# Kernel optimization log

Hardware: AMD Instinct MI355X
Metric: run time of the kernel (lower is better)

Reference implementation:

```python
import jax, jax.numpy as jnp
import numpy as np

# Config (matches init_kwargs)
HIDDEN = 1280
NUM_EXPERTS = 16
NUM_SHARED = 2
NUM_ROUTED = NUM_EXPERTS - NUM_SHARED          # 14
TOPK = 6 - NUM_SHARED                           # num_activated - num_shared = 4
INTERMED = int(int(HIDDEN * 4.0) * 0.25)        # 1280
B, S = 2, 2048


def setup_inputs() -> dict:
    key = jax.random.key(0)
    ks = jax.random.split(key, 12)
    sc = 0.02
    x = jax.random.normal(ks[0], (B, S, HIDDEN), dtype=jnp.float32)
    # shared experts, stacked over expert axis
    W1s = jax.random.normal(ks[1], (NUM_SHARED, HIDDEN, INTERMED), dtype=jnp.float32) * sc
    b1s = jnp.zeros((NUM_SHARED, INTERMED), dtype=jnp.float32)
    W2s = jax.random.normal(ks[2], (NUM_SHARED, INTERMED, HIDDEN), dtype=jnp.float32) * sc
    b2s = jnp.zeros((NUM_SHARED, HIDDEN), dtype=jnp.float32)
    # routed experts
    W1r = jax.random.normal(ks[3], (NUM_ROUTED, HIDDEN, INTERMED), dtype=jnp.float32) * sc
    b1r = jnp.zeros((NUM_ROUTED, INTERMED), dtype=jnp.float32)
    W2r = jax.random.normal(ks[4], (NUM_ROUTED, INTERMED, HIDDEN), dtype=jnp.float32) * sc
    b2r = jnp.zeros((NUM_ROUTED, HIDDEN), dtype=jnp.float32)
    # router
    Wr = jax.random.normal(ks[5], (HIDDEN, NUM_ROUTED), dtype=jnp.float32) * sc
    br = jnp.zeros((NUM_ROUTED,), dtype=jnp.float32)
    return {"x": x, "W1s": W1s, "b1s": b1s, "W2s": W2s, "b2s": b2s,
            "W1r": W1r, "b1r": b1r, "W2r": W2r, "b2r": b2r, "Wr": Wr, "br": br}


def _gelu(x):
    return jax.nn.gelu(x, approximate=False)  # torch nn.GELU default is exact erf


def reference(x, W1s, b1s, W2s, b2s, W1r, b1r, W2r, b2r, Wr, br):
    # shared experts: sum_e FFN_e(x)
    hs = _gelu(jnp.einsum('bsh,ehi->ebsi', x, W1s) + b1s[:, None, None, :])
    shared_out = jnp.einsum('ebsi,eih->bsh', hs, W2s) + b2s.sum(0)

    # router: softmax + top-k gates scattered back to dense [B,S,E]
    logits = jnp.einsum('bsh,he->bse', x, Wr) + br
    aff = jax.nn.softmax(logits, axis=-1)
    topk_vals, topk_idx = jax.lax.top_k(aff, TOPK)
    gates = (jax.nn.one_hot(topk_idx, NUM_ROUTED, dtype=aff.dtype)
             * topk_vals[..., None]).sum(axis=-2)  # [B,S,E]

    # naive dense dispatch: every routed expert over all tokens, gate-weighted
    hr = _gelu(jnp.einsum('bsh,ehi->ebsi', x, W1r) + b1r[:, None, None, :])
    expert_out = jnp.einsum('ebsi,eih->ebsh', hr, W2r) + b2r[:, None, None, :]
    routed_out = jnp.einsum('bse,ebsh->bsh', gates, expert_out)

    return shared_out + routed_out + x
```

## Files before the change

kernel.cpp:

```cpp
#include <hip/hip_runtime.h>
#include <hip/hip_bf16.h>
#include <math.h>

#define H      1280
#define NE     16
#define NR     14
#define TK     4
#define T      4096
#define NROWS  24576
#define MAXT   112
#define NT     (H / 64)

typedef __bf16 bf16x8 __attribute__((ext_vector_type(8)));
typedef float  f32x4  __attribute__((ext_vector_type(4)));
typedef unsigned short us8 __attribute__((ext_vector_type(8)));

__device__ __forceinline__ unsigned short f2bf(float f) {
  unsigned int u = __float_as_uint(f);
  u += 0x7fffu + ((u >> 16) & 1u);
  return (unsigned short)(u >> 16);
}
__device__ __forceinline__ float bf2f(unsigned short u) {
  return __uint_as_float(((unsigned int)u) << 16);
}

__device__ __forceinline__ void gll16(const unsigned short* g, unsigned short* l) {
  __builtin_amdgcn_global_load_lds(
      (const __attribute__((address_space(1))) void*)g,
      (__attribute__((address_space(3))) void*)l, 16, 0, 0);
}

__global__ void k_init(int* cnt, int* fill) {
  int i = threadIdx.x;
  if (i < 16) { cnt[i] = 0; fill[i] = 0; }
}

__global__ void k_cast_x(const float* __restrict__ x, unsigned short* __restrict__ xb) {
  int i = blockIdx.x * 256 + threadIdx.x;
  float4 v = reinterpret_cast<const float4*>(x)[i];
  ushort4 b;
  b.x = f2bf(v.x); b.y = f2bf(v.y); b.z = f2bf(v.z); b.w = f2bf(v.w);
  reinterpret_cast<ushort4*>(xb)[i] = b;
}

__global__ void k_transpose(const float* __restrict__ W1s, const float* __restrict__ W2s,
                            const float* __restrict__ W1r, const float* __restrict__ W2r,
                            unsigned short* __restrict__ w1b, unsigned short* __restrict__ w2b) {
  int mat = blockIdx.z;
  int fam = mat >> 4;
  int e   = mat & 15;
  size_t msz = (size_t)H * H;
  const float* src;
  unsigned short* dst;
  if (fam == 0) {
    src = (e < 2) ? W1s + (size_t)e * msz : W1r + (size_t)(e - 2) * msz;
    dst = w1b + (size_t)e * msz;
  } else {
    src = (e < 2) ? W2s + (size_t)e * msz : W2r + (size_t)(e - 2) * msz;
    dst = w2b + (size_t)e * msz;
  }
  __shared__ unsigned short tile[64][72];
  int tx = threadIdx.x & 15;
  int ty = threadIdx.x >> 4;
  int bx = blockIdx.x * 64;
  int by = blockIdx.y * 64;
#pragma unroll
  for (int p = 0; p < 4; p++) {
    int r = p * 16 + ty;
    float4 v = *reinterpret_cast<const float4*>(&src[(size_t)(by + r) * H + bx + tx * 4]);
    tile[tx * 4 + 0][r] = f2bf(v.x);
    tile[tx * 4 + 1][r] = f2bf(v.y);
    tile[tx * 4 + 2][r] = f2bf(v.z);
    tile[tx * 4 + 3][r] = f2bf(v.w);
  }
  __syncthreads();
  int tx8 = threadIdx.x & 7;
  int rr  = threadIdx.x >> 3;
#pragma unroll
  for (int p = 0; p < 2; p++) {
    int n = p * 32 + rr;
    us8 o = *reinterpret_cast<const us8*>(&tile[n][tx8 * 8]);
    *reinterpret_cast<us8*>(&dst[(size_t)(bx + n) * H + by + tx8 * 8]) = o;
  }
}

__global__ void k_router(const float* __restrict__ x, const float* __restrict__ Wr,
                         const float* __restrict__ br,
                         int* __restrict__ topk_e, float* __restrict__ topk_g) {
  int t  = blockIdx.x * 4 + (threadIdx.x >> 6);
  int ln = threadIdx.x & 63;
  float part[NR];
#pragma unroll
  for (int e = 0; e < NR; e++) part[e] = 0.f;
  const float* xr = x + (size_t)t * H;
  for (int k = ln; k < H; k += 64) {
    float xv = xr[k];
    const float* w = Wr + (size_t)k * NR;
#pragma unroll
    for (int e = 0; e < NR; e++) part[e] += xv * w[e];
  }
  float aff[NR];
#pragma unroll
  for (int e = 0; e < NR; e++) {
    float v = part[e];
#pragma unroll
    for (int off = 32; off; off >>= 1) v += __shfl_down(v, off);
    aff[e] = v + br[e];
  }
  if (ln == 0) {
    float mx = aff[0];
#pragma unroll
    for (int e = 1; e < NR; e++) mx = fmaxf(mx, aff[e]);
    float p[NR]; float s = 0.f;
#pragma unroll
    for (int e = 0; e < NR; e++) { p[e] = expf(aff[e] - mx); s += p[e]; }
    float inv = 1.f / s;
    unsigned used = 0;
    for (int j = 0; j < TK; j++) {
      int be = -1; float bv = -1.f;
#pragma unroll
      for (int e = 0; e < NR; e++)
        if (!((used >> e) & 1u) && p[e] > bv) { bv = p[e]; be = e; }
      used |= 1u << be;
      topk_e[t * TK + j] = be;
      topk_g[t * TK + j] = bv * inv;
    }
  }
}

__global__ void k_count(const int* __restrict__ topk_e, int* __restrict__ cnt) {
  __shared__ int hist[NR];
  int tid = threadIdx.x;
  if (tid < NR) hist[tid] = 0;
  __syncthreads();
  int t = blockIdx.x * 256 + tid;
#pragma unroll
  for (int j = 0; j < TK; j++)
    atomicAdd(&hist[topk_e[t * TK + j]], 1);
  __syncthreads();
  if (tid < NR) atomicAdd(&cnt[tid], hist[tid]);
}

__global__ void k_prefix(const int* __restrict__ cnt, int* __restrict__ segbase,
                         int* __restrict__ segcnt, int* __restrict__ tile_seg,
                         int* __restrict__ tile_m0) {
  if (threadIdx.x == 0) {
    int sc[NE];
    sc[0] = T; sc[1] = T;
    for (int e = 0; e < NR; e++) sc[2 + e] = cnt[e];
    int b = 0;
    for (int s = 0; s < NE; s++) { segbase[s] = b; segcnt[s] = sc[s]; b += sc[s]; }
    int nt = 0;
    for (int s = 0; s < NE; s++)
      for (int m = 0; m < sc[s]; m += 256) { tile_seg[nt] = s; tile_m0[nt] = m; nt++; }
    for (int i = nt; i < MAXT; i++) { tile_seg[i] = -1; tile_m0[i] = 0; }
  }
}

__global__ void k_fill(const int* __restrict__ topk_e,
                       const int* __restrict__ segbase, int* __restrict__ fill,
                       int* __restrict__ rowtok, int* __restrict__ tokrow) {
  __shared__ int lhist[NR];
  __shared__ int lbase[NR];
  int tid = threadIdx.x;
  if (tid < NR) lhist[tid] = 0;
  __syncthreads();
  int t = blockIdx.x * 256 + tid;
  rowtok[t]     = t;
  rowtok[T + t] = t;
  int e[TK], off[TK];
#pragma unroll
  for (int j = 0; j < TK; j++) {
    e[j]   = topk_e[t * TK + j];
    off[j] = atomicAdd(&lhist[e[j]], 1);
  }
  __syncthreads();
  if (tid < NR) lbase[tid] = atomicAdd(&fill[tid], lhist[tid]);
  __syncthreads();
#pragma unroll
  for (int j = 0; j < TK; j++) {
    int r = segbase[2 + e[j]] + lbase[e[j]] + off[j];
    rowtok[r] = t;
    tokrow[t * TK + j] = r;
  }
}


template<int MODE>
__global__ __launch_bounds__(512, 2) void k_gemm(
    const unsigned short* __restrict__ Abase,
    const unsigned short* __restrict__ Wb,
    const float* __restrict__ bs, const float* __restrict__ brr,
    const int* __restrict__ rowtok,
    const int* __restrict__ segbase, const int* __restrict__ segcnt,
    const int* __restrict__ tile_seg, const int* __restrict__ tile_m0,
    unsigned short* __restrict__ obuf) {
  int seg = tile_seg[blockIdx.y];
  if (seg < 0) return;
  int m0  = tile_m0[blockIdx.y];
  int cnt = segcnt[seg];
  int n0  = blockIdx.x * 256;
  int sb  = segbase[seg];
  const unsigned short* Bw = Wb + (size_t)seg * H * H;
  const float* bias = (seg < 2) ? bs + (size_t)seg * H : brr + (size_t)(seg - 2) * H;

  __shared__ __align__(16) unsigned short Al[2][256 * 64];
  __shared__ __align__(16) unsigned short Bl[2][256 * 64];

  int tid = threadIdx.x;
  int wv = tid >> 6, ln = tid & 63;
  int rw = (wv & 1) * 128, cw = (wv >> 1) * 64;
  int quad = ln >> 4, l16 = ln & 15;
  int lrow = tid >> 3;
  int ldst = (tid & 7) * 8;
  int lkc  = (((tid & 7) ^ (lrow & 7))) * 8;

  const unsigned short* asrc[4];
  const unsigned short* bsrc[4];
#pragma unroll
  for (int p = 0; p < 4; p++) {
    int row = p * 64 + lrow;
    if (MODE == 0) {
      int gm  = m0 + row;
      int tok = (gm < cnt) ? rowtok[sb + gm] : 0;
      asrc[p] = Abase + (size_t)tok * H + lkc;
    } else {
      int ar = sb + m0 + row;
      if (ar >= NROWS) ar = 0;
      asrc[p] = Abase + (size_t)ar * H + lkc;
    }
    bsrc[p] = Bw + (size_t)(n0 + row) * H + lkc;
  }

  int xsw = (quad ^ (l16 & 7)) * 8;

  f32x4 acc[8][4];
#pragma unroll
  for (int i = 0; i < 8; i++)
#pragma unroll
    for (int j = 0; j < 4; j++) acc[i][j] = (f32x4){0.f, 0.f, 0.f, 0.f};

  auto STAGE = [&](int tt) {
    int kb = tt << 6;
    unsigned short* Ad = &Al[tt & 1][0];
    unsigned short* Bd = &Bl[tt & 1][0];
#pragma unroll
    for (int p = 0; p < 4; p++) {
      int row = p * 64 + lrow;
      gll16(asrc[p] + kb, Ad + row * 64 + ldst);
      gll16(bsrc[p] + kb, Bd + row * 64 + ldst);
    }
  };

  STAGE(0);
  __syncthreads();

  for (int t = 0; t < NT; ++t) {
    if (t + 1 < NT) STAGE(t + 1);
    const unsigned short* Ac = &Al[t & 1][0];
    const unsigned short* Bc = &Bl[t & 1][0];
#pragma unroll
    for (int kk = 0; kk < 64; kk += 32) {
      bf16x8 af[8], bfr[4];
#pragma unroll
      for (int i = 0; i < 8; i++)
        af[i] = *reinterpret_cast<const bf16x8*>(&Ac[(rw + i * 16 + l16) * 64 + (xsw ^ kk)]);
#pragma unroll
      for (int j = 0; j < 4; j++)
        bfr[j] = *reinterpret_cast<const bf16x8*>(&Bc[(cw + j * 16 + l16) * 64 + (xsw ^ kk)]);
#pragma unroll
      for (int i = 0; i < 8; i++)
#pragma unroll
        for (int j = 0; j < 4; j++)
          acc[i][j] = __builtin_amdgcn_mfma_f32_16x16x32_bf16(af[i], bfr[j], acc[i][j], 0, 0, 0);
    }
    __syncthreads();
  }

#pragma unroll
  for (int i = 0; i < 8; i++) {
#pragma unroll
    for (int r = 0; r < 4; r++) {
      int m = m0 + rw + i * 16 + quad * 4 + r;
      if (m >= cnt) continue;
      size_t ro = (size_t)(sb + m) * H;
#pragma unroll
      for (int j = 0; j < 4; j++) {
        int n = n0 + cw + j * 16 + l16;
        float v = acc[i][j][r] + bias[n];
        if (MODE == 0) {
          float g = 0.5f * v * (1.f + erff(v * 0.70710678118654752f));
          obuf[ro + n] = f2bf(g);
        } else {
          obuf[ro + n] = f2bf(v);
        }
      }
    }
  }
}

__global__ void k_combine(const float* __restrict__ x, const unsigned short* __restrict__ rbuf,
                          const int* __restrict__ tokrow, const float* __restrict__ topk_g,
                          float* __restrict__ out) {
  int i = blockIdx.x * 256 + threadIdx.x;
  int t = i / (H / 4);
  int c = (i - t * (H / 4)) * 4;
  size_t xo = (size_t)t * H + c;
  float4 acc = *reinterpret_cast<const float4*>(&x[xo]);
  {
    ushort4 u0 = *reinterpret_cast<const ushort4*>(&rbuf[(size_t)t * H + c]);
    ushort4 u1 = *reinterpret_cast<const ushort4*>(&rbuf[(size_t)(T + t) * H + c]);
    acc.x += bf2f(u0.x) + bf2f(u1.x);
    acc.y += bf2f(u0.y) + bf2f(u1.y);
    acc.z += bf2f(u0.z) + bf2f(u1.z);
    acc.w += bf2f(u0.w) + bf2f(u1.w);
  }
#pragma unroll
  for (int j = 0; j < TK; j++) {
    int r   = tokrow[t * TK + j];
    float g = topk_g[t * TK + j];
    ushort4 u = *reinterpret_cast<const ushort4*>(&rbuf[(size_t)r * H + c]);
    acc.x += g * bf2f(u.x);
    acc.y += g * bf2f(u.y);
    acc.z += g * bf2f(u.z);
    acc.w += g * bf2f(u.w);
  }
  *reinterpret_cast<float4*>(&out[xo]) = acc;
}

extern "C" void kernel_launch(void* const* d_in, const int* in_sizes, int n_in,
                              void* d_out, int out_size, void* d_ws, size_t ws_size,
                              hipStream_t stream) {
  const float* x   = (const float*)d_in[0];
  const float* W1s = (const float*)d_in[1];
  const float* b1s = (const float*)d_in[2];
  const float* W2s = (const float*)d_in[3];
  const float* b2s = (const float*)d_in[4];
  const float* W1r = (const float*)d_in[5];
  const float* b1r = (const float*)d_in[6];
  const float* W2r = (const float*)d_in[7];
  const float* b2r = (const float*)d_in[8];
  const float* Wr  = (const float*)d_in[9];
  const float* br  = (const float*)d_in[10];
  float* out = (float*)d_out;

  char* ws = (char*)d_ws;
  const size_t SZ_XB = (size_t)T * H * 2;
  const size_t SZ_WB = (size_t)NE * H * H * 2;
  const size_t SZ_H  = (size_t)NROWS * H * 2;
  size_t off = 0;
  unsigned short* xb   = (unsigned short*)(ws + off); off += SZ_XB;
  unsigned short* w1b  = (unsigned short*)(ws + off); off += SZ_WB;
  unsigned short* w2b  = (unsigned short*)(ws + off); off += SZ_WB;
  unsigned short* hbuf = (unsigned short*)(ws + off); off += SZ_H;
  int*   rowtok  = (int*)(ws + off);   off += NROWS * 4;
  int*   tokrow  = (int*)(ws + off);   off += T * TK * 4;
  int*   topk_e  = (int*)(ws + off);   off += T * TK * 4;
  float* topk_g  = (float*)(ws + off); off += T * TK * 4;
  int*   cnt     = (int*)(ws + off);   off += 64;
  int*   fill    = (int*)(ws + off);   off += 64;
  int*   segbase = (int*)(ws + off);   off += 64;
  int*   segcnt  = (int*)(ws + off);   off += 64;
  int*   tile_seg = (int*)(ws + off);  off += MAXT * 4;
  int*   tile_m0  = (int*)(ws + off);  off += MAXT * 4;
  unsigned short* rbuf = (unsigned short*)ws;

  hipLaunchKernelGGL(k_init, dim3(1), dim3(64), 0, stream, cnt, fill);
  hipLaunchKernelGGL(k_cast_x, dim3((T * H / 4) / 256), dim3(256), 0, stream, x, xb);
  hipLaunchKernelGGL(k_transpose, dim3(20, 20, 32), dim3(256), 0, stream,
                     W1s, W2s, W1r, W2r, w1b, w2b);
  hipLaunchKernelGGL(k_router, dim3(T / 4), dim3(256), 0, stream, x, Wr, br, topk_e, topk_g);
  hipLaunchKernelGGL(k_count, dim3(T / 256), dim3(256), 0, stream, topk_e, cnt);
  hipLaunchKernelGGL(k_prefix, dim3(1), dim3(1), 0, stream, cnt, segbase, segcnt, tile_seg, tile_m0);
  hipLaunchKernelGGL(k_fill, dim3(T / 256), dim3(256), 0, stream,
                     topk_e, segbase, fill, rowtok, tokrow);
  hipLaunchKernelGGL(HIP_KERNEL_NAME(k_gemm<0>), dim3(5, MAXT, 1), dim3(512), 0, stream,
                     xb, w1b, b1s, b1r, rowtok, segbase, segcnt, tile_seg, tile_m0, hbuf);
  hipLaunchKernelGGL(HIP_KERNEL_NAME(k_gemm<1>), dim3(5, MAXT, 1), dim3(512), 0, stream,
                     hbuf, w2b, b2s, b2r, rowtok, segbase, segcnt, tile_seg, tile_m0, rbuf);
  hipLaunchKernelGGL(k_combine, dim3((T * H / 4) / 256), dim3(256), 0, stream,
                     x, rbuf, tokrow, topk_g, out);
}
```

Baseline: 587.8 us.

## Shrink grouped GEMM tiles to 128x128, drop double buffering, fuse x cast into router

The grouped expert GEMMs move from 256x256 tiles with 512 threads and double-buffered LDS to 128x128 tiles with 256 threads and a single LDS buffer, raising the maximum tile count and the grid width. The aim is more, smaller blocks and less padding waste on the per-expert row segments, with more blocks resident per CU. The separate x-to-bf16 cast kernel is removed; the router now writes the bf16 copy of x while it reads x. In exchange, loads are no longer overlapped with MFMA work and each tile reuses its data less, and the router's bf16 stores are strided scalar writes.

```diff
diff --git a/kernel.cpp b/kernel.cpp
--- a/kernel.cpp
+++ b/kernel.cpp
@@ -8,7 +8,7 @@
 #define TK     4
 #define T      4096
 #define NROWS  24576
-#define MAXT   112
+#define MAXT   208
 #define NT     (H / 64)
 
 typedef __bf16 bf16x8 __attribute__((ext_vector_type(8)));
@@ -33,14 +33,6 @@
 __global__ void k_init(int* cnt, int* fill) {
   int i = threadIdx.x;
   if (i < 16) { cnt[i] = 0; fill[i] = 0; }
-}
-
-__global__ void k_cast_x(const float* __restrict__ x, unsigned short* __restrict__ xb) {
-  int i = blockIdx.x * 256 + threadIdx.x;
-  float4 v = reinterpret_cast<const float4*>(x)[i];
-  ushort4 b;
-  b.x = f2bf(v.x); b.y = f2bf(v.y); b.z = f2bf(v.z); b.w = f2bf(v.w);
-  reinterpret_cast<ushort4*>(xb)[i] = b;
 }
 
 __global__ void k_transpose(const float* __restrict__ W1s, const float* __restrict__ W2s,
@@ -86,15 +78,18 @@
 
 __global__ void k_router(const float* __restrict__ x, const float* __restrict__ Wr,
                          const float* __restrict__ br,
-                         int* __restrict__ topk_e, float* __restrict__ topk_g) {
+                         int* __restrict__ topk_e, float* __restrict__ topk_g,
+                         unsigned short* __restrict__ xb) {
   int t  = blockIdx.x * 4 + (threadIdx.x >> 6);
   int ln = threadIdx.x & 63;
   float part[NR];
 #pragma unroll
   for (int e = 0; e < NR; e++) part[e] = 0.f;
   const float* xr = x + (size_t)t * H;
+  unsigned short* xw = xb + (size_t)t * H;
   for (int k = ln; k < H; k += 64) {
     float xv = xr[k];
+    xw[k] = f2bf(xv);
     const float* w = Wr + (size_t)k * NR;
 #pragma unroll
     for (int e = 0; e < NR; e++) part[e] += xv * w[e];
@@ -152,7 +147,7 @@
     for (int s = 0; s < NE; s++) { segbase[s] = b; segcnt[s] = sc[s]; b += sc[s]; }
     int nt = 0;
     for (int s = 0; s < NE; s++)
-      for (int m = 0; m < sc[s]; m += 256) { tile_seg[nt] = s; tile_m0[nt] = m; nt++; }
+      for (int m = 0; m < sc[s]; m += 128) { tile_seg[nt] = s; tile_m0[nt] = m; nt++; }
     for (int i = nt; i < MAXT; i++) { tile_seg[i] = -1; tile_m0[i] = 0; }
   }
 }
@@ -187,7 +182,7 @@
 
 
 template<int MODE>
-__global__ __launch_bounds__(512, 2) void k_gemm(
+__global__ __launch_bounds__(256, 3) void k_gemm(
     const unsigned short* __restrict__ Abase,
     const unsigned short* __restrict__ Wb,
     const float* __restrict__ bs, const float* __restrict__ brr,
@@ -199,17 +194,17 @@
   if (seg < 0) return;
   int m0  = tile_m0[blockIdx.y];
   int cnt = segcnt[seg];
-  int n0  = blockIdx.x * 256;
+  int n0  = blockIdx.x * 128;
   int sb  = segbase[seg];
   const unsigned short* Bw = Wb + (size_t)seg * H * H;
   const float* bias = (seg < 2) ? bs + (size_t)seg * H : brr + (size_t)(seg - 2) * H;
 
-  __shared__ __align__(16) unsigned short Al[2][256 * 64];
-  __shared__ __align__(16) unsigned short Bl[2][256 * 64];
+  __shared__ __align__(16) unsigned short Al[128 * 64];
+  __shared__ __align__(16) unsigned short Bl[128 * 64];
 
   int tid = threadIdx.x;
   int wv = tid >> 6, ln = tid & 63;
-  int rw = (wv & 1) * 128, cw = (wv >> 1) * 64;
+  int rw = (wv & 1) * 64, cw = (wv >> 1) * 64;
   int quad = ln >> 4, l16 = ln & 15;
   int lrow = tid >> 3;
   int ldst = (tid & 7) * 8;
@@ -219,7 +214,7 @@
   const unsigned short* bsrc[4];
 #pragma unroll
   for (int p = 0; p < 4; p++) {
-    int row = p * 64 + lrow;
+    int row = p * 32 + lrow;
     if (MODE == 0) {
       int gm  = m0 + row;
       int tok = (gm < cnt) ? rowtok[sb + gm] : 0;
@@ -234,51 +229,40 @@
 
   int xsw = (quad ^ (l16 & 7)) * 8;
 
-  f32x4 acc[8][4];
-#pragma unroll
-  for (int i = 0; i < 8; i++)
+  f32x4 acc[4][4];
+#pragma unroll
+  for (int i = 0; i < 4; i++)
 #pragma unroll
     for (int j = 0; j < 4; j++) acc[i][j] = (f32x4){0.f, 0.f, 0.f, 0.f};
 
-  auto STAGE = [&](int tt) {
-    int kb = tt << 6;
-    unsigned short* Ad = &Al[tt & 1][0];
-    unsigned short* Bd = &Bl[tt & 1][0];
+  for (int k0 = 0; k0 < H; k0 += 64) {
+    __syncthreads();
 #pragma unroll
     for (int p = 0; p < 4; p++) {
-      int row = p * 64 + lrow;
-      gll16(asrc[p] + kb, Ad + row * 64 + ldst);
-      gll16(bsrc[p] + kb, Bd + row * 64 + ldst);
-    }
-  };
-
-  STAGE(0);
-  __syncthreads();
-
-  for (int t = 0; t < NT; ++t) {
-    if (t + 1 < NT) STAGE(t + 1);
-    const unsigned short* Ac = &Al[t & 1][0];
-    const unsigned short* Bc = &Bl[t & 1][0];
+      int row = p * 32 + lrow;
+      gll16(asrc[p] + k0, &Al[row * 64 + ldst]);
+      gll16(bsrc[p] + k0, &Bl[row * 64 + ldst]);
+    }
+    __syncthreads();
 #pragma unroll
     for (int kk = 0; kk < 64; kk += 32) {
-      bf16x8 af[8], bfr[4];
-#pragma unroll
-      for (int i = 0; i < 8; i++)
-        af[i] = *reinterpret_cast<const bf16x8*>(&Ac[(rw + i * 16 + l16) * 64 + (xsw ^ kk)]);
+      bf16x8 af[4], bfr[4];
+#pragma unroll
+      for (int i = 0; i < 4; i++)
+        af[i] = *reinterpret_cast<const bf16x8*>(&Al[(rw + i * 16 + l16) * 64 + (xsw ^ kk)]);
 #pragma unroll
       for (int j = 0; j < 4; j++)
-        bfr[j] = *reinterpret_cast<const bf16x8*>(&Bc[(cw + j * 16 + l16) * 64 + (xsw ^ kk)]);
-#pragma unroll
-      for (int i = 0; i < 8; i++)
+        bfr[j] = *reinterpret_cast<const bf16x8*>(&Bl[(cw + j * 16 + l16) * 64 + (xsw ^ kk)]);
+#pragma unroll
+      for (int i = 0; i < 4; i++)
 #pragma unroll
         for (int j = 0; j < 4; j++)
           acc[i][j] = __builtin_amdgcn_mfma_f32_16x16x32_bf16(af[i], bfr[j], acc[i][j], 0, 0, 0);
     }
-    __syncthreads();
-  }
-
-#pragma unroll
-  for (int i = 0; i < 8; i++) {
+  }
+
+#pragma unroll
+  for (int i = 0; i < 4; i++) {
 #pragma unroll
     for (int r = 0; r < 4; r++) {
       int m = m0 + rw + i * 16 + quad * 4 + r;
@@ -366,17 +350,16 @@
   unsigned short* rbuf = (unsigned short*)ws;
 
   hipLaunchKernelGGL(k_init, dim3(1), dim3(64), 0, stream, cnt, fill);
-  hipLaunchKernelGGL(k_cast_x, dim3((T * H / 4) / 256), dim3(256), 0, stream, x, xb);
   hipLaunchKernelGGL(k_transpose, dim3(20, 20, 32), dim3(256), 0, stream,
                      W1s, W2s, W1r, W2r, w1b, w2b);
-  hipLaunchKernelGGL(k_router, dim3(T / 4), dim3(256), 0, stream, x, Wr, br, topk_e, topk_g);
+  hipLaunchKernelGGL(k_router, dim3(T / 4), dim3(256), 0, stream, x, Wr, br, topk_e, topk_g, xb);
   hipLaunchKernelGGL(k_count, dim3(T / 256), dim3(256), 0, stream, topk_e, cnt);
   hipLaunchKernelGGL(k_prefix, dim3(1), dim3(1), 0, stream, cnt, segbase, segcnt, tile_seg, tile_m0);
   hipLaunchKernelGGL(k_fill, dim3(T / 256), dim3(256), 0, stream,
                      topk_e, segbase, fill, rowtok, tokrow);
-  hipLaunchKernelGGL(HIP_KERNEL_NAME(k_gemm<0>), dim3(5, MAXT, 1), dim3(512), 0, stream,
+  hipLaunchKernelGGL(HIP_KERNEL_NAME(k_gemm<0>), dim3(10, MAXT, 1), dim3(256), 0, stream,
                      xb, w1b, b1s, b1r, rowtok, segbase, segcnt, tile_seg, tile_m0, hbuf);
-  hipLaunchKernelGGL(HIP_KERNEL_NAME(k_gemm<1>), dim3(5, MAXT, 1), dim3(512), 0, stream,
+  hipLaunchKernelGGL(HIP_KERNEL_NAME(k_gemm<1>), dim3(10, MAXT, 1), dim3(256), 0, stream,
                      hbuf, w2b, b2s, b2r, rowtok, segbase, segcnt, tile_seg, tile_m0, rbuf);
   hipLaunchKernelGGL(k_combine, dim3((T * H / 4) / 256), dim3(256), 0, stream,
                      x, rbuf, tokrow, topk_g, out);
```

Result: no change. 582.7 us (-0.9%).
